# Kernel tuning notes

Measured on AMD Instinct MI355X. Metric: run time of the kernel, lower is better.

The kernel has to match this reference:

```python
import jax, jax.numpy as jnp
import numpy as np

EPS = 1e-5
NEG = -1e9

def rmsnorm(x, g, eps=EPS):
    x32 = x.astype(jnp.float32)
    n = x32 * jax.lax.rsqrt(jnp.mean(x32 * x32, axis=-1, keepdims=True) + eps)
    return g * n.astype(x.dtype)

def setup_inputs() -> dict:
    key = jax.random.key(0)
    ks = jax.random.split(key, 10)
    B, S, D, H = 2, 2048, 768, 12
    F = 4 * D
    s = 0.02
    return {
        "x": jax.random.normal(ks[0], (B, S, D), jnp.float32),
        "mask": jax.random.randint(ks[1], (B, S, S), 0, 2, jnp.int32),
        "wq": jax.random.normal(ks[2], (D, D), jnp.float32) * s,
        "wk": jax.random.normal(ks[3], (D, D), jnp.float32) * s,
        "wv": jax.random.normal(ks[4], (D, D), jnp.float32) * s,
        "wo": jax.random.normal(ks[5], (D, D), jnp.float32) * s,
        "w1": jax.random.normal(ks[6], (F, D), jnp.float32) * s,
        "w2": jax.random.normal(ks[7], (D, F), jnp.float32) * s,
        "w3": jax.random.normal(ks[8], (F, D), jnp.float32) * s,
        "g_attn": jnp.ones((D,), jnp.float32),
        "g_ffn": jnp.ones((D,), jnp.float32),
    }

def reference(x, mask, wq, wk, wv, wo, w1, w2, w3, g_attn, g_ffn):
    B, S, D = x.shape
    H = 12
    Dk = D // H
    # --- attention sub-block (pre-norm) ---
    xn = rmsnorm(x, g_attn)
    # torch Linear: y = x @ W^T; split heads -> [B,H,S,Dk]
    q = (xn @ wq.T).reshape(B, S, H, Dk).transpose(0, 2, 1, 3)
    k = (xn @ wk.T).reshape(B, S, H, Dk).transpose(0, 2, 1, 3)
    v = (xn @ wv.T).reshape(B, S, H, Dk).transpose(0, 2, 1, 3)
    scores = jnp.einsum("bhqd,bhkd->bhqk", q, k) / jnp.sqrt(jnp.float32(Dk))
    scores = jnp.where(mask[:, None, :, :] == 0, jnp.float32(NEG), scores)
    probs = jax.nn.softmax(scores, axis=-1)  # dropout p=0.0 -> identity
    attn = jnp.einsum("bhqk,bhkd->bhqd", probs, v)
    attn = attn.transpose(0, 2, 1, 3).reshape(B, S, D)
    h = x + attn @ wo.T
    # --- SwiGLU FFN sub-block (pre-norm) ---
    hn = rmsnorm(h, g_ffn)
    ffn = (jax.nn.silu(hn @ w1.T) * (hn @ w3.T)) @ w2.T
    return h + ffn
```

## Files before the change

kernel.cpp:

```cpp
#include <hip/hip_runtime.h>
#include <hip/hip_bf16.h>

#define S_LEN 2048
#define D_MODEL 768
#define NH 12
#define DK 64
#define F_DIM 3072
#define BATCH 2
#define M_ROWS (BATCH * S_LEN)

typedef __bf16 bf16x8 __attribute__((ext_vector_type(8)));
typedef float floatx4 __attribute__((ext_vector_type(4)));
typedef unsigned short u16;
typedef unsigned long long u64;

__device__ inline float bf2f(u16 u) {
    union { unsigned int i; float f; } x; x.i = ((unsigned int)u) << 16; return x.f;
}
__device__ inline u16 f2bf(float f) {
    union { float f; unsigned int i; } x; x.f = f;
    unsigned int r = x.i + 0x7fffu + ((x.i >> 16) & 1u);
    return (u16)(r >> 16);
}
__device__ __forceinline__ bf16x8 as_bf16x8(uint4 v) {
    union { uint4 u; bf16x8 b; } c; c.u = v; return c.b;
}

__device__ __forceinline__ void ldsload16(const u16* g, u16* l) {
    __builtin_amdgcn_global_load_lds(
        (const __attribute__((address_space(1))) unsigned int*)g,
        (__attribute__((address_space(3))) unsigned int*)l, 16, 0, 0);
}

__global__ __launch_bounds__(256)
void cvt_all(const float4* __restrict__ wq, const float4* __restrict__ wk,
             const float4* __restrict__ wv, const float4* __restrict__ wo,
             const float4* __restrict__ w1, const float4* __restrict__ w2,
             const float4* __restrict__ w3,
             ushort4* wqb, ushort4* wkb, ushort4* wvb, ushort4* wob,
             ushort4* w13f, ushort4* w2b) {
    const int WS4 = (D_MODEL * D_MODEL) / 4;
    const int WB4 = (F_DIM * D_MODEL) / 4;
    const int RW4 = D_MODEL / 4;
    int i = blockIdx.x * 256 + threadIdx.x;
    const float4* src; ushort4* dst; int off, doff;
    if (i < 4 * WS4) {
        int s = i / WS4; off = i - s * WS4; doff = off;
        src = (s == 0) ? wq : (s == 1) ? wk : (s == 2) ? wv : wo;
        dst = (s == 0) ? wqb : (s == 1) ? wkb : (s == 2) ? wvb : wob;
    } else {
        int j = i - 4 * WS4; int s = j / WB4; off = j - s * WB4;
        if (s == 1) { src = w2; dst = w2b; doff = off; }
        else {
            src = (s == 0) ? w1 : w3;
            dst = w13f;
            int which = (s == 0) ? 0 : 1;
            int row = off / RW4, c4 = off - row * RW4;
            int k = c4 * 4;
            int n_tile = row >> 4, nl = row & 15;
            int k_tile = k >> 5, quad = (k >> 3) & 3, jj = k & 7;
            int lane = quad * 16 + nl;
            int f = (n_tile * 24 + k_tile) * 2 + which;
            doff = (f * 512 + lane * 8 + jj) >> 2;
        }
    }
    float4 v = src[off];
    ushort4 o;
    o.x = f2bf(v.x); o.y = f2bf(v.y); o.z = f2bf(v.z); o.w = f2bf(v.w);
    dst[doff] = o;
}

__global__ __launch_bounds__(256)
void mask_bits(const int* __restrict__ m, u64* __restrict__ bits) {
    size_t gid = (size_t)blockIdx.x * 256 + threadIdx.x;
    u64 b = __ballot(m[gid] != 0);
    if ((threadIdx.x & 63) == 0) bits[gid >> 6] = b;
}

__global__ __launch_bounds__(256)
void rmsnorm_k(const float* __restrict__ x, const float* __restrict__ g, u16* __restrict__ out) {
    int row = blockIdx.x;
    const float* xr = x + (size_t)row * D_MODEL;
    u16* orow = out + (size_t)row * D_MODEL;
    int t = threadIdx.x;
    float v0 = xr[t];
    float v1 = xr[t + 256];
    float v2 = xr[t + 512];
    float ss = v0 * v0 + v1 * v1 + v2 * v2;
    #pragma unroll
    for (int off = 1; off < 64; off <<= 1) ss += __shfl_xor(ss, off);
    __shared__ float red[4];
    if ((t & 63) == 0) red[t >> 6] = ss;
    __syncthreads();
    float tot = red[0] + red[1] + red[2] + red[3];
    float scale = rsqrtf(tot * (1.0f / (float)D_MODEL) + 1e-5f);
    orow[t]       = f2bf(g[t]       * v0 * scale);
    orow[t + 256] = f2bf(g[t + 256] * v1 * scale);
    orow[t + 512] = f2bf(g[t + 512] * v2 * scale);
}

__global__ __launch_bounds__(256, 3)
void gemm_f1(const u16* __restrict__ A, const u16* __restrict__ W13f,
             u16* __restrict__ Cout) {
    const int K = D_MODEL, N = F_DIM;
    __shared__ u16 As[2][64][32];

    int t = threadIdx.x;
    int w = t >> 6, lane = t & 63;
    int lrow = lane & 15, quad = lane >> 4;

    int lid = blockIdx.y * 24 + blockIdx.x;
    int xcd = lid & 7, s = lid >> 3;
    int nb = xcd * 3 + (s % 3);
    int mb = s / 3;
    int mBase = mb * 64;
    int ntile0 = nb * 8 + w * 2;

    int srow = lane >> 2;
    int scolS = ((lane & 3) ^ ((lane >> 3) & 3)) * 8;
    int rq = (quad ^ ((lrow >> 1) & 3)) * 8;
    const u16* Ag = A + (size_t)(mBase + w * 16 + srow) * K + scolS;
    const uint4* Bf = (const uint4*)W13f;

    auto stageA = [&](int k0, int b) {
        ldsload16(Ag + k0, &As[b][w * 16][0]);
    };

    floatx4 zero = {0.f, 0.f, 0.f, 0.f};
    floatx4 acc[4][2], acc2[4][2];
    #pragma unroll
    for (int r = 0; r < 4; ++r)
        #pragma unroll
        for (int c = 0; c < 2; ++c) { acc[r][c] = zero; acc2[r][c] = zero; }

    stageA(0, 0);
    int cur = 0;
    for (int kt = 0; kt < 24; ++kt) {
        uint4 b1v[2], b3v[2];
        #pragma unroll
        for (int c = 0; c < 2; ++c) {
            int f = ((ntile0 + c) * 24 + kt) * 2;
            b1v[c] = Bf[(size_t)f * 64 + lane];
            b3v[c] = Bf[(size_t)(f + 1) * 64 + lane];
        }
        __syncthreads();
        if (kt + 1 < 24) stageA((kt + 1) * 32, cur ^ 1);

        bf16x8 af[4];
        #pragma unroll
        for (int r = 0; r < 4; ++r) af[r] = *(const bf16x8*)&As[cur][r * 16 + lrow][rq];
        #pragma unroll
        for (int c = 0; c < 2; ++c) {
            bf16x8 b1f = as_bf16x8(b1v[c]);
            bf16x8 b3f = as_bf16x8(b3v[c]);
            #pragma unroll
            for (int r = 0; r < 4; ++r) {
                acc[r][c]  = __builtin_amdgcn_mfma_f32_16x16x32_bf16(af[r], b1f, acc[r][c], 0, 0, 0);
                acc2[r][c] = __builtin_amdgcn_mfma_f32_16x16x32_bf16(af[r], b3f, acc2[r][c], 0, 0, 0);
            }
        }
        cur ^= 1;
    }

    #pragma unroll
    for (int r = 0; r < 4; ++r) {
        #pragma unroll
        for (int c = 0; c < 2; ++c) {
            #pragma unroll
            for (int j = 0; j < 4; ++j) {
                int grow = mBase + r * 16 + quad * 4 + j;
                int gcol = nb * 128 + w * 32 + c * 16 + lrow;
                float a = acc[r][c][j];
                Cout[(size_t)grow * N + gcol] = f2bf((a / (1.0f + __expf(-a))) * acc2[r][c][j]);
            }
        }
    }
}

__global__ __launch_bounds__(256, 3)
void gemm64(const u16* __restrict__ A, const u16* __restrict__ B1,
            const float* __restrict__ R, float* __restrict__ Cout, int N, int K) {
    __shared__ u16 As[2][64][64];
    __shared__ u16 Bs[2][64][64];

    int t = threadIdx.x;
    int w = t >> 6, lane = t & 63;
    int mBase = blockIdx.y * 64, nBase = blockIdx.x * 64;
    int lrow = lane & 15, quad = lane >> 4;
    int wm = (w >> 1) * 32, wn = (w & 1) * 32;

    int srow8 = lane >> 3;
    int sc64 = ((lane & 7) ^ srow8) * 8;
    const u16* Ag = A  + (size_t)(mBase + w * 16 + srow8) * K + sc64;
    const u16* Bg = B1 + (size_t)(nBase + w * 16 + srow8) * K + sc64;

    auto stage = [&](int k0, int b) {
        ldsload16(Ag + k0,                 &As[b][w * 16][0]);
        ldsload16(Ag + (size_t)8 * K + k0, &As[b][w * 16 + 8][0]);
        ldsload16(Bg + k0,                 &Bs[b][w * 16][0]);
        ldsload16(Bg + (size_t)8 * K + k0, &Bs[b][w * 16 + 8][0]);
    };

    floatx4 zero = {0.f, 0.f, 0.f, 0.f};
    floatx4 acc[2][2];
    #pragma unroll
    for (int r = 0; r < 2; ++r)
        #pragma unroll
        for (int c = 0; c < 2; ++c) acc[r][c] = zero;

    stage(0, 0);
    int cur = 0;
    for (int k0 = 0; k0 < K; k0 += 64) {
        __syncthreads();
        if (k0 + 64 < K) stage(k0 + 64, cur ^ 1);

        #pragma unroll
        for (int half = 0; half < 2; ++half) {
            int rc = ((half * 4 + quad) ^ (lrow & 7)) * 8;
            bf16x8 af[2], bf[2];
            #pragma unroll
            for (int r = 0; r < 2; ++r) af[r] = *(const bf16x8*)&As[cur][wm + r * 16 + lrow][rc];
            #pragma unroll
            for (int c = 0; c < 2; ++c) bf[c] = *(const bf16x8*)&Bs[cur][wn + c * 16 + lrow][rc];
            #pragma unroll
            for (int r = 0; r < 2; ++r)
                #pragma unroll
                for (int c = 0; c < 2; ++c)
                    acc[r][c] = __builtin_amdgcn_mfma_f32_16x16x32_bf16(af[r], bf[c], acc[r][c], 0, 0, 0);
        }
        cur ^= 1;
    }

    #pragma unroll
    for (int r = 0; r < 2; ++r) {
        #pragma unroll
        for (int c = 0; c < 2; ++c) {
            #pragma unroll
            for (int j = 0; j < 4; ++j) {
                int grow = mBase + wm + r * 16 + quad * 4 + j;
                int gcol = nBase + wn + c * 16 + lrow;
                size_t idx = (size_t)grow * N + gcol;
                Cout[idx] = acc[r][c][j] + R[idx];
            }
        }
    }
}

__global__ __launch_bounds__(256, 4)
void gemm_qkv(const u16* __restrict__ A, const u16* __restrict__ wq,
              const u16* __restrict__ wk, const u16* __restrict__ wv,
              u16* __restrict__ qb, u16* __restrict__ kb, u16* __restrict__ vt) {
    const int K = D_MODEL;
    __shared__ u16 As[2][64][32];
    __shared__ u16 Bs[2][128][32];

    int t = threadIdx.x;
    int w = t >> 6, lane = t & 63;
    int nb = blockIdx.x;
    int which = nb / 6;
    int mBase = blockIdx.y * 64, nBase = (nb % 6) * 128;
    const u16* B1 = (which == 0) ? wq : (which == 1) ? wk : wv;
    int lrow = lane & 15, quad = lane >> 4;
    int wm = (w >> 1) * 32, wn = (w & 1) * 64;

    int srow = lane >> 2;
    int scolS = ((lane & 3) ^ ((lane >> 3) & 3)) * 8;
    int rq = (quad ^ ((lrow >> 1) & 3)) * 8;
    const u16* Ag = A  + (size_t)(mBase + w * 16 + srow) * K + scolS;
    const u16* Bg = B1 + (size_t)(nBase + w * 32 + srow) * K + scolS;

    auto stage = [&](int k0, int b) {
        ldsload16(Ag + k0, &As[b][w * 16][0]);
        ldsload16(Bg + k0, &Bs[b][w * 32][0]);
        ldsload16(Bg + (size_t)16 * K + k0, &Bs[b][w * 32 + 16][0]);
    };

    floatx4 zero = {0.f, 0.f, 0.f, 0.f};
    floatx4 acc[2][4];
    #pragma unroll
    for (int r = 0; r < 2; ++r)
        #pragma unroll
        for (int c = 0; c < 4; ++c) acc[r][c] = zero;

    stage(0, 0);
    int cur = 0;
    for (int k0 = 0; k0 < K; k0 += 32) {
        __syncthreads();
        if (k0 + 32 < K) stage(k0 + 32, cur ^ 1);
        bf16x8 af[2];
        #pragma unroll
        for (int r = 0; r < 2; ++r) af[r] = *(const bf16x8*)&As[cur][wm + r * 16 + lrow][rq];
        #pragma unroll
        for (int c = 0; c < 4; ++c) {
            bf16x8 bfr = *(const bf16x8*)&Bs[cur][wn + c * 16 + lrow][rq];
            #pragma unroll
            for (int r = 0; r < 2; ++r)
                acc[r][c] = __builtin_amdgcn_mfma_f32_16x16x32_bf16(af[r], bfr, acc[r][c], 0, 0, 0);
        }
        cur ^= 1;
    }

    u16* dst = (which == 0) ? qb : kb;
    const float qscale = 0.18033688011112042f;
    #pragma unroll
    for (int r = 0; r < 2; ++r) {
        #pragma unroll
        for (int c = 0; c < 4; ++c) {
            #pragma unroll
            for (int j = 0; j < 4; ++j) {
                int grow = mBase + wm + r * 16 + quad * 4 + j;
                int gcol = nBase + wn + c * 16 + lrow;
                float val = acc[r][c][j];
                if (which == 2) {
                    int bb = grow >> 11, s = grow & 2047;
                    int hh = gcol >> 6, d = gcol & 63;
                    vt[((((size_t)bb * NH + hh) * DK + d) << 11) + s] = f2bf(val);
                } else {
                    if (which == 0) val *= qscale;
                    dst[(size_t)grow * D_MODEL + gcol] = f2bf(val);
                }
            }
        }
    }
}

__global__ __launch_bounds__(256)
void attn_mfma(const u16* __restrict__ q, const u16* __restrict__ k,
               const u16* __restrict__ vt, const u64* __restrict__ mbits,
               u16* __restrict__ out) {
    __shared__ u16 Ks0[2][64][32], Ks1[2][64][32];
    __shared__ u16 Vs0[2][64][32], Vs1[2][64][32];
    __shared__ u16 PT[4][16][72];

    int t = threadIdx.x;
    int lane = t & 63;
    int w = t >> 6;
    int lrow = lane & 15;
    int quad = lane >> 4;

    int st0 = blockIdx.x * 64;
    int bh = blockIdx.y;
    int h = bh % NH;
    int b = bh / NH;

    const u16* kbase = k + (size_t)b * S_LEN * D_MODEL + h * DK;
    const u16* vbase = vt + (size_t)bh * DK * S_LEN;
    const u64* bw = mbits + ((size_t)b * S_LEN + st0 + w * 16 + lrow) * (S_LEN / 64);

    int srow = lane >> 2;
    int scolS = ((lane & 3) ^ ((lane >> 3) & 3)) * 8;
    int rq = (quad ^ ((lrow >> 1) & 3)) * 8;

    const u16* kg = kbase + (size_t)(w * 16 + srow) * D_MODEL + scolS;
    const u16* vg = vbase + (size_t)(w * 16 + srow) * S_LEN + scolS;

    auto stageKV = [&](int kt, int bsel) {
        ldsload16(kg + (size_t)kt * D_MODEL,      &Ks0[bsel][w * 16][0]);
        ldsload16(kg + (size_t)kt * D_MODEL + 32, &Ks1[bsel][w * 16][0]);
        ldsload16(vg + kt,      &Vs0[bsel][w * 16][0]);
        ldsload16(vg + kt + 32, &Vs1[bsel][w * 16][0]);
    };

    stageKV(0, 0);

    bf16x8 bq0, bq1;
    {
        const u16* qrow = q + ((size_t)b * S_LEN + st0 + w * 16 + lrow) * D_MODEL + h * DK + quad * 8;
        bq0 = *(const bf16x8*)qrow;
        bq1 = *(const bf16x8*)(qrow + 32);
    }

    bf16x8 ones;
    {
        union { u16 u; __bf16 b; } o; o.u = 0x3F80;
        #pragma unroll
        for (int j = 0; j < 8; ++j) ones[j] = o.b;
    }

    floatx4 zero = {0.f, 0.f, 0.f, 0.f};
    floatx4 Ot[4] = {zero, zero, zero, zero};
    floatx4 Osum = zero;

    u64 mw = bw[0];
    __syncthreads();

    int cur = 0;
    for (int kt = 0; kt < S_LEN; kt += 64) {
        if (kt + 64 < S_LEN) stageKV(kt + 64, cur ^ 1);
        u64 mw_next = (kt + 64 < S_LEN) ? bw[(kt >> 6) + 1] : 0ull;
        unsigned mlo = (unsigned)mw, mhi = (unsigned)(mw >> 32);

        floatx4 st[4];
        #pragma unroll
        for (int nt = 0; nt < 4; ++nt) {
            bf16x8 ak0 = *(const bf16x8*)&Ks0[cur][nt * 16 + lrow][rq];
            bf16x8 ak1 = *(const bf16x8*)&Ks1[cur][nt * 16 + lrow][rq];
            st[nt] = __builtin_amdgcn_mfma_f32_16x16x32_bf16(ak0, bq0, zero, 0, 0, 0);
            st[nt] = __builtin_amdgcn_mfma_f32_16x16x32_bf16(ak1, bq1, st[nt], 0, 0, 0);
        }

        #pragma unroll
        for (int nt = 0; nt < 4; ++nt) {
            unsigned half = (nt & 2) ? mhi : mlo;
            unsigned tmp = half >> ((nt & 1) * 16 + quad * 4);
            unsigned eu[4];
            #pragma unroll
            for (int j = 0; j < 4; ++j) {
                float e = __builtin_amdgcn_exp2f(st[nt][j]);
                unsigned msk = (unsigned)((int)(tmp << (31 - j)) >> 31);
                eu[j] = __float_as_uint(e) & msk;
            }
            uint2 p;
            p.x = (eu[0] >> 16) | (eu[1] & 0xffff0000u);
            p.y = (eu[2] >> 16) | (eu[3] & 0xffff0000u);
            *(uint2*)&PT[w][lrow][nt * 16 + quad * 4] = p;
        }

        bf16x8 ap0 = *(const bf16x8*)&PT[w][lrow][quad * 8];
        bf16x8 ap1 = *(const bf16x8*)&PT[w][lrow][32 + quad * 8];
        Osum = __builtin_amdgcn_mfma_f32_16x16x32_bf16(ap0, ones, Osum, 0, 0, 0);
        Osum = __builtin_amdgcn_mfma_f32_16x16x32_bf16(ap1, ones, Osum, 0, 0, 0);
        #pragma unroll
        for (int dt = 0; dt < 4; ++dt) {
            bf16x8 bv0 = *(const bf16x8*)&Vs0[cur][dt * 16 + lrow][rq];
            bf16x8 bv1 = *(const bf16x8*)&Vs1[cur][dt * 16 + lrow][rq];
            Ot[dt] = __builtin_amdgcn_mfma_f32_16x16x32_bf16(ap0, bv0, Ot[dt], 0, 0, 0);
            Ot[dt] = __builtin_amdgcn_mfma_f32_16x16x32_bf16(ap1, bv1, Ot[dt], 0, 0, 0);
        }

        __syncthreads();
        cur ^= 1;
        mw = mw_next;
    }

    float invj[4];
    #pragma unroll
    for (int j = 0; j < 4; ++j) invj[j] = 1.0f / Osum[j];

    u16* obase = out + ((size_t)b * S_LEN + st0 + w * 16) * D_MODEL + h * DK;
    #pragma unroll
    for (int dt = 0; dt < 4; ++dt)
        #pragma unroll
        for (int j = 0; j < 4; ++j)
            obase[(size_t)(quad * 4 + j) * D_MODEL + dt * 16 + lrow] = f2bf(Ot[dt][j] * invj[j]);
}

extern "C" void kernel_launch(void* const* d_in, const int* in_sizes, int n_in,
                              void* d_out, int out_size, void* d_ws, size_t ws_size,
                              hipStream_t stream) {
    const float* x      = (const float*)d_in[0];
    const int*   mask   = (const int*)d_in[1];
    const float* wq     = (const float*)d_in[2];
    const float* wk     = (const float*)d_in[3];
    const float* wv     = (const float*)d_in[4];
    const float* wo     = (const float*)d_in[5];
    const float* w1     = (const float*)d_in[6];
    const float* w2     = (const float*)d_in[7];
    const float* w3     = (const float*)d_in[8];
    const float* g_attn = (const float*)d_in[9];
    const float* g_ffn  = (const float*)d_in[10];
    float* out = (float*)d_out;

    const size_t WSMALL = (size_t)D_MODEL * D_MODEL;
    const size_t WBIG   = (size_t)F_DIM * D_MODEL;
    const size_t MD     = (size_t)M_ROWS * D_MODEL;

    char* ws = (char*)d_ws;
    u16* wqb  = (u16*)ws;            ws += WSMALL * 2;
    u16* wkb  = (u16*)ws;            ws += WSMALL * 2;
    u16* wvb  = (u16*)ws;            ws += WSMALL * 2;
    u16* wob  = (u16*)ws;            ws += WSMALL * 2;
    u16* w13f = (u16*)ws;            ws += WBIG * 2 * 2;
    u16* w2b  = (u16*)ws;            ws += WBIG * 2;
    u16* xn  = (u16*)ws;             ws += MD * 2;
    u16* qb  = (u16*)ws;             ws += MD * 2;
    u16* kb  = (u16*)ws;             ws += MD * 2;
    u16* vb  = (u16*)ws;             ws += MD * 2;
    u16* ao  = (u16*)ws;             ws += MD * 2;
    float* hb = (float*)ws;          ws += MD * 4;
    u64* mb  = (u64*)ws;             ws += (size_t)BATCH * S_LEN * (S_LEN / 64) * 8;
    u16* hn = xn;
    u16* ub = qb;
    (void)ws_size; (void)n_in; (void)in_sizes; (void)out_size;

    dim3 blk(256);

    cvt_all<<<9216, blk, 0, stream>>>((const float4*)wq, (const float4*)wk, (const float4*)wv,
                                      (const float4*)wo, (const float4*)w1, (const float4*)w2,
                                      (const float4*)w3,
                                      (ushort4*)wqb, (ushort4*)wkb, (ushort4*)wvb, (ushort4*)wob,
                                      (ushort4*)w13f, (ushort4*)w2b);
    mask_bits<<<(BATCH * S_LEN * S_LEN) / 256, blk, 0, stream>>>(mask, mb);

    rmsnorm_k<<<M_ROWS, blk, 0, stream>>>(x, g_attn, xn);
    gemm_qkv<<<dim3(18, M_ROWS / 64), blk, 0, stream>>>(xn, wqb, wkb, wvb, qb, kb, vb);
    attn_mfma<<<dim3(S_LEN / 64, BATCH * NH), blk, 0, stream>>>(qb, kb, vb, mb, ao);
    gemm64<<<dim3(D_MODEL / 64, M_ROWS / 64), blk, 0, stream>>>(ao, wob, x, hb, D_MODEL, D_MODEL);
    rmsnorm_k<<<M_ROWS, blk, 0, stream>>>((const float*)hb, g_ffn, hn);
    gemm_f1<<<dim3(24, M_ROWS / 64), blk, 0, stream>>>(hn, w13f, ub);
    gemm64<<<dim3(D_MODEL / 64, M_ROWS / 64), blk, 0, stream>>>(ub, w2b, hb, out, D_MODEL, F_DIM);
}
```

Measured before the change: 332.8 us.

## Deepen gemm_f1 K-step to 64 and add XCD-aware block remapping

gemm_f1 now stages 64-wide K slices of A per barrier with an 8-way XOR swizzle, halving the number of sync iterations and loading two B fragment sets per step. gemm64, gemm_qkv and attn_mfma remap their linear block IDs so that consecutive blocks landing on the same XCD cover neighbouring tiles, which should improve L2 reuse of shared operands. The remaps hardcode grid shapes (64 M-tiles, 18x64 and 32x24 grids), and the larger A tile raises LDS use and register pressure in gemm_f1.

```diff
diff --git a/kernel.cpp b/kernel.cpp
--- a/kernel.cpp
+++ b/kernel.cpp
@@ -103,7 +103,7 @@
 void gemm_f1(const u16* __restrict__ A, const u16* __restrict__ W13f,
              u16* __restrict__ Cout) {
     const int K = D_MODEL, N = F_DIM;
-    __shared__ u16 As[2][64][32];
+    __shared__ u16 As[2][64][64];
 
     int t = threadIdx.x;
     int w = t >> 6, lane = t & 63;
@@ -116,14 +116,14 @@
     int mBase = mb * 64;
     int ntile0 = nb * 8 + w * 2;
 
-    int srow = lane >> 2;
-    int scolS = ((lane & 3) ^ ((lane >> 3) & 3)) * 8;
-    int rq = (quad ^ ((lrow >> 1) & 3)) * 8;
-    const u16* Ag = A + (size_t)(mBase + w * 16 + srow) * K + scolS;
+    int srow8 = lane >> 3;
+    int sc64 = ((lane & 7) ^ srow8) * 8;
+    const u16* Ag = A + (size_t)(mBase + w * 16 + srow8) * K + sc64;
     const uint4* Bf = (const uint4*)W13f;
 
     auto stageA = [&](int k0, int b) {
-        ldsload16(Ag + k0, &As[b][w * 16][0]);
+        ldsload16(Ag + k0,                 &As[b][w * 16][0]);
+        ldsload16(Ag + (size_t)8 * K + k0, &As[b][w * 16 + 8][0]);
     };
 
     floatx4 zero = {0.f, 0.f, 0.f, 0.f};
@@ -135,28 +135,36 @@
 
     stageA(0, 0);
     int cur = 0;
-    for (int kt = 0; kt < 24; ++kt) {
-        uint4 b1v[2], b3v[2];
-        #pragma unroll
-        for (int c = 0; c < 2; ++c) {
-            int f = ((ntile0 + c) * 24 + kt) * 2;
-            b1v[c] = Bf[(size_t)f * 64 + lane];
-            b3v[c] = Bf[(size_t)(f + 1) * 64 + lane];
+    for (int kt2 = 0; kt2 < 12; ++kt2) {
+        uint4 b1v[2][2], b3v[2][2];
+        #pragma unroll
+        for (int hh = 0; hh < 2; ++hh) {
+            int kt = kt2 * 2 + hh;
+            #pragma unroll
+            for (int c = 0; c < 2; ++c) {
+                int f = ((ntile0 + c) * 24 + kt) * 2;
+                b1v[hh][c] = Bf[(size_t)f * 64 + lane];
+                b3v[hh][c] = Bf[(size_t)(f + 1) * 64 + lane];
+            }
         }
         __syncthreads();
-        if (kt + 1 < 24) stageA((kt + 1) * 32, cur ^ 1);
-
-        bf16x8 af[4];
-        #pragma unroll
-        for (int r = 0; r < 4; ++r) af[r] = *(const bf16x8*)&As[cur][r * 16 + lrow][rq];
-        #pragma unroll
-        for (int c = 0; c < 2; ++c) {
-            bf16x8 b1f = as_bf16x8(b1v[c]);
-            bf16x8 b3f = as_bf16x8(b3v[c]);
-            #pragma unroll
-            for (int r = 0; r < 4; ++r) {
-                acc[r][c]  = __builtin_amdgcn_mfma_f32_16x16x32_bf16(af[r], b1f, acc[r][c], 0, 0, 0);
-                acc2[r][c] = __builtin_amdgcn_mfma_f32_16x16x32_bf16(af[r], b3f, acc2[r][c], 0, 0, 0);
+        if (kt2 + 1 < 12) stageA((kt2 + 1) * 64, cur ^ 1);
+
+        #pragma unroll
+        for (int hh = 0; hh < 2; ++hh) {
+            int rc = ((hh * 4 + quad) ^ (lrow & 7)) * 8;
+            bf16x8 af[4];
+            #pragma unroll
+            for (int r = 0; r < 4; ++r) af[r] = *(const bf16x8*)&As[cur][r * 16 + lrow][rc];
+            #pragma unroll
+            for (int c = 0; c < 2; ++c) {
+                bf16x8 b1f = as_bf16x8(b1v[hh][c]);
+                bf16x8 b3f = as_bf16x8(b3v[hh][c]);
+                #pragma unroll
+                for (int r = 0; r < 4; ++r) {
+                    acc[r][c]  = __builtin_amdgcn_mfma_f32_16x16x32_bf16(af[r], b1f, acc[r][c], 0, 0, 0);
+                    acc2[r][c] = __builtin_amdgcn_mfma_f32_16x16x32_bf16(af[r], b3f, acc2[r][c], 0, 0, 0);
+                }
             }
         }
         cur ^= 1;
@@ -185,7 +193,13 @@
 
     int t = threadIdx.x;
     int w = t >> 6, lane = t & 63;
-    int mBase = blockIdx.y * 64, nBase = blockIdx.x * 64;
+
+    int L = blockIdx.y * gridDim.x + blockIdx.x;
+    int per = (gridDim.x * 64) >> 3;
+    int g = (L & 7) * per + (L >> 3);
+    int mBase = (g & 63) * 64;
+    int nBase = (g >> 6) * 64;
+
     int lrow = lane & 15, quad = lane >> 4;
     int wm = (w >> 1) * 32, wn = (w & 1) * 32;
 
@@ -256,9 +270,13 @@
 
     int t = threadIdx.x;
     int w = t >> 6, lane = t & 63;
-    int nb = blockIdx.x;
-    int which = nb / 6;
-    int mBase = blockIdx.y * 64, nBase = (nb % 6) * 128;
+
+    int L = blockIdx.y * 18 + blockIdx.x;
+    int g = (L & 7) * 144 + (L >> 3);
+    int xI = g >> 6;
+    int yI = g & 63;
+    int which = xI / 6;
+    int mBase = yI * 64, nBase = (xI % 6) * 128;
     const u16* B1 = (which == 0) ? wq : (which == 1) ? wk : wv;
     int lrow = lane & 15, quad = lane >> 4;
     int wm = (w >> 1) * 32, wn = (w & 1) * 64;
@@ -338,8 +356,10 @@
     int lrow = lane & 15;
     int quad = lane >> 4;
 
-    int st0 = blockIdx.x * 64;
-    int bh = blockIdx.y;
+    int L = blockIdx.y * gridDim.x + blockIdx.x;
+    int g = (L & 7) * 96 + (L >> 3);
+    int st0 = (g & 31) * 64;
+    int bh = g >> 5;
     int h = bh % NH;
     int b = bh / NH;
 
```

After: 333.5 us. About the same (+0.2%).
